# Optimization experiments

Hardware: AMD Instinct MI355X
Metric: run time of the kernel (lower is better)

The kernel has to match this reference:

```python
import jax, jax.numpy as jnp
import numpy as np


def setup_inputs() -> dict:
    key = jax.random.key(0)
    ks = jax.random.split(key, 7)
    B, T, H, O = 2048, 2048, 32, 2
    SCALE = 0.1  # keep gates out of deep saturation
    return {
        "x": jax.random.normal(ks[0], (B, T), dtype=jnp.float32),
        "w_ih": jax.random.normal(ks[1], (3 * H, 1), dtype=jnp.float32) * SCALE,
        "w_hh": jax.random.normal(ks[2], (3 * H, H), dtype=jnp.float32) * SCALE,
        "b_ih": jax.random.normal(ks[3], (3 * H,), dtype=jnp.float32) * SCALE,
        "b_hh": jax.random.normal(ks[4], (3 * H,), dtype=jnp.float32) * SCALE,
        "head_w": jax.random.normal(ks[5], (O, H), dtype=jnp.float32) * SCALE,
        "head_b": jax.random.normal(ks[6], (O,), dtype=jnp.float32) * SCALE,
    }


def reference(x, w_ih, w_hh, b_ih, b_hh, head_w, head_b):
    # x: [B, T] scalar time series (torch does x.unsqueeze(-1)).
    B, T = x.shape
    H = w_hh.shape[1]
    # Precompute input contributions to all 3 gates: [B, T, 3H]
    # (input_size == 1, so this is an outer product with w_ih[:, 0]).
    xg = x[:, :, None] * w_ih[:, 0] + b_ih
    xg_t = jnp.swapaxes(xg, 0, 1)  # [T, B, 3H] for scan

    def step(h, xg_step):
        gh = h @ w_hh.T + b_hh  # [B, 3H]
        xr, xz, xn = jnp.split(xg_step, 3, axis=-1)
        hr, hz, hn = jnp.split(gh, 3, axis=-1)
        r = jax.nn.sigmoid(xr + hr)
        z = jax.nn.sigmoid(xz + hz)
        n = jnp.tanh(xn + r * hn)
        h_new = (1.0 - z) * n + z * h
        return h_new, None

    h0 = jnp.zeros((B, H), dtype=x.dtype)
    hT, _ = jax.lax.scan(step, h0, xg_t)
    # head applied to last timestep's output (== final hidden state)
    return hT @ head_w.T + head_b
```

## Files before the change

### kernel.cpp

```cpp
#include <hip/hip_runtime.h>


typedef _Float16 f16x2 __attribute__((ext_vector_type(2)));

__device__ __forceinline__ float fdot2(int a, int b, float c) {
    return __builtin_amdgcn_fdot2(__builtin_bit_cast(f16x2, a),
                                  __builtin_bit_cast(f16x2, b), c, false);
}

__device__ __forceinline__ int pack_pair(float a, float b) {
    f16x2 p;
    p.x = (_Float16)a;
    p.y = (_Float16)b;
    return __builtin_bit_cast(int, p);
}

__global__ __launch_bounds__(64, 1)
void gru_scan_kernel(const float* __restrict__ x,
                     const float* __restrict__ w_ih,
                     const float* __restrict__ w_hh,
                     const float* __restrict__ b_ih,
                     const float* __restrict__ b_hh,
                     const float* __restrict__ head_w,
                     const float* __restrict__ head_b,
                     float* __restrict__ out,
                     int T)
{
    const int l = (int)threadIdx.x;
    const int g = l >> 5;
    const int j = l & 31;
    const int b = (int)blockIdx.x * 2 + g;

    __shared__ __align__(16) _Float16 h16[2][32];
    __shared__ float hf_s[2][32];
    __shared__ __align__(16) float x_s[2][2][32];

    const float NL2E  = -1.44269504088896f;
    const float P2L2E =  2.88539008177793f;

    int wR[16], wZ[16], wN[16];
    {
        const float* pR = w_hh + (     j) * 32;
        const float* pZ = w_hh + (32 + j) * 32;
        const float* pN = w_hh + (64 + j) * 32;
#pragma unroll
        for (int q = 0; q < 16; ++q) {
            wR[q] = pack_pair(NL2E  * pR[2*q], NL2E  * pR[2*q+1]);
            wZ[q] = pack_pair(NL2E  * pZ[2*q], NL2E  * pZ[2*q+1]);
            wN[q] = pack_pair(P2L2E * pN[2*q], P2L2E * pN[2*q+1]);
        }
    }
#pragma unroll
    for (int q = 0; q < 16; ++q) {
        asm volatile("" : "+v"(wR[q]), "+v"(wZ[q]), "+v"(wN[q]));
    }

    const float wihr = NL2E  * w_ih[j];
    const float wihz = NL2E  * w_ih[32 + j];
    const float wihn = P2L2E * w_ih[64 + j];
    const float br   = NL2E  * (b_ih[j]      + b_hh[j]);
    const float bz   = NL2E  * (b_ih[32 + j] + b_hh[32 + j]);
    const float bni  = P2L2E * b_ih[64 + j];
    const float bnh  = P2L2E * b_hh[64 + j];

    const float* xrow   = x + (size_t)b * (size_t)T;
    const int    nchunk = T >> 5;

    float h = 0.0f;
    h16[g][j]    = (_Float16)0.0f;
    x_s[g][0][j] = xrow[j];
    float xnext  = (nchunk > 1) ? xrow[32 + j] : 0.0f;
    __builtin_amdgcn_wave_barrier();

    const int4* hq = (const int4*)(&h16[g][0]);

    for (int c = 0; c < nchunk; ++c) {
        const int buf = c & 1;
        const float* xs = &x_s[g][buf][0];
#pragma unroll 4
        for (int s = 0; s < 32; ++s) {
            const float xv = xs[s];
            const int4 H0 = hq[0];
            const int4 H1 = hq[1];
            const int4 H2 = hq[2];
            const int4 H3 = hq[3];
            const float hm1 = h - 1.0f;

            float rA = fdot2(H0.x, wR[ 0], fmaf(xv, wihr, br));
            float rB = fdot2(H1.x, wR[ 4], 0.0f);
            float rC = fdot2(H2.x, wR[ 8], 0.0f);
            float rD = fdot2(H3.x, wR[12], 0.0f);
            rA = fdot2(H0.y, wR[ 1], rA); rB = fdot2(H1.y, wR[ 5], rB);
            rC = fdot2(H2.y, wR[ 9], rC); rD = fdot2(H3.y, wR[13], rD);
            rA = fdot2(H0.z, wR[ 2], rA); rB = fdot2(H1.z, wR[ 6], rB);
            rC = fdot2(H2.z, wR[10], rC); rD = fdot2(H3.z, wR[14], rD);
            rA = fdot2(H0.w, wR[ 3], rA); rB = fdot2(H1.w, wR[ 7], rB);
            rC = fdot2(H2.w, wR[11], rC); rD = fdot2(H3.w, wR[15], rD);
            const float er = __builtin_amdgcn_exp2f((rA + rB) + (rC + rD));
            const float r  = __builtin_amdgcn_rcpf(1.0f + er);

            float zA = fdot2(H0.x, wZ[ 0], fmaf(xv, wihz, bz));
            float zB = fdot2(H1.x, wZ[ 4], 0.0f);
            float zC = fdot2(H2.x, wZ[ 8], 0.0f);
            float zD = fdot2(H3.x, wZ[12], 0.0f);
            zA = fdot2(H0.y, wZ[ 1], zA); zB = fdot2(H1.y, wZ[ 5], zB);
            zC = fdot2(H2.y, wZ[ 9], zC); zD = fdot2(H3.y, wZ[13], zD);
            zA = fdot2(H0.z, wZ[ 2], zA); zB = fdot2(H1.z, wZ[ 6], zB);
            zC = fdot2(H2.z, wZ[10], zC); zD = fdot2(H3.z, wZ[14], zD);
            zA = fdot2(H0.w, wZ[ 3], zA); zB = fdot2(H1.w, wZ[ 7], zB);
            zC = fdot2(H2.w, wZ[11], zC); zD = fdot2(H3.w, wZ[15], zD);
            const float ez    = __builtin_amdgcn_exp2f((zA + zB) + (zC + zD));
            const float z     = __builtin_amdgcn_rcpf(1.0f + ez);
            const float m2omz = fmaf(2.0f, z, -2.0f);
            const float ohz   = fmaf(z, hm1, 1.0f);

            float nA = fdot2(H0.x, wN[ 0], bnh);
            float nB = fdot2(H1.x, wN[ 4], 0.0f);
            float nC = fdot2(H2.x, wN[ 8], 0.0f);
            float nD = fdot2(H3.x, wN[12], 0.0f);
            nA = fdot2(H0.y, wN[ 1], nA); nB = fdot2(H1.y, wN[ 5], nB);
            nC = fdot2(H2.y, wN[ 9], nC); nD = fdot2(H3.y, wN[13], nD);
            nA = fdot2(H0.z, wN[ 2], nA); nB = fdot2(H1.z, wN[ 6], nB);
            nC = fdot2(H2.z, wN[10], nC); nD = fdot2(H3.z, wN[14], nD);
            nA = fdot2(H0.w, wN[ 3], nA); nB = fdot2(H1.w, wN[ 7], nB);
            nC = fdot2(H2.w, wN[11], nC); nD = fdot2(H3.w, wN[15], nD);
            const float np = (nA + nB) + (nC + nD);
            const float u  = fmaf(r, np, fmaf(xv, wihn, bni));
            const float et = __builtin_amdgcn_exp2f(u);
            const float ti = __builtin_amdgcn_rcpf(1.0f + et);
            h = fmaf(m2omz, ti, ohz);

            __builtin_amdgcn_wave_barrier();
            h16[g][j] = (_Float16)h;
            __builtin_amdgcn_wave_barrier();
        }
        if (c + 1 < nchunk) {
            x_s[g][1 - buf][j] = xnext;
            if (c + 2 < nchunk) xnext = xrow[(c + 2) * 32 + j];
            __builtin_amdgcn_wave_barrier();
        }
    }

    hf_s[g][j] = h;
    __builtin_amdgcn_wave_barrier();
    if (l < 4) {
        const int g2 = l >> 1, o = l & 1;
        float acc = head_b[o];
        const float* hw = head_w + o * 32;
#pragma unroll
        for (int k = 0; k < 32; ++k) acc = fmaf(hf_s[g2][k], hw[k], acc);
        out[((int)blockIdx.x * 2 + g2) * 2 + o] = acc;
    }
}

extern "C" void kernel_launch(void* const* d_in, const int* in_sizes, int n_in,
                              void* d_out, int out_size, void* d_ws, size_t ws_size,
                              hipStream_t stream) {
    const float* x      = (const float*)d_in[0];
    const float* w_ih   = (const float*)d_in[1];
    const float* w_hh   = (const float*)d_in[2];
    const float* b_ih   = (const float*)d_in[3];
    const float* b_hh   = (const float*)d_in[4];
    const float* head_w = (const float*)d_in[5];
    const float* head_b = (const float*)d_in[6];
    float* out = (float*)d_out;

    const int B = out_size / 2;
    const int T = in_sizes[0] / B;

    dim3 grid(B / 2), block(64);
    hipLaunchKernelGGL(gru_scan_kernel, grid, block, 0, stream,
                       x, w_ih, w_hh, b_ih, b_hh, head_w, head_b, out, T);
}
```

Before: 526.3 us.

## Broadcast hidden state via permlane32_swap and DPP instead of LDS

Replaces the per-step LDS store and reload of the fp16 hidden state with register exchange. permlane32_swap pairs each lane's h with its partner half-wave, and a tree of DPP row permutes builds the 16 packed h pairs each lane needs. Lanes are remapped so the two batch elements interleave in 16-lane groups, and weight pairs are permuted at setup to match the DPP order. The aim is to cut LDS latency and the wave barriers from the serial recurrence critical path, at the cost of 16 extra DPP moves per step and fragile lane-mapping logic.

```diff
diff --git a/kernel.cpp b/kernel.cpp
--- a/kernel.cpp
+++ b/kernel.cpp
@@ -15,6 +15,11 @@
     return __builtin_bit_cast(int, p);
 }
 
+template<int CTRL>
+__device__ __forceinline__ int dppmov(int src) {
+    return __builtin_amdgcn_update_dpp(0, src, CTRL, 0xF, 0xF, true);
+}
+
 __global__ __launch_bounds__(64, 1)
 void gru_scan_kernel(const float* __restrict__ x,
                      const float* __restrict__ w_ih,
@@ -26,28 +31,40 @@
                      float* __restrict__ out,
                      int T)
 {
-    const int l = (int)threadIdx.x;
-    const int g = l >> 5;
-    const int j = l & 31;
-    const int b = (int)blockIdx.x * 2 + g;
+    const int l  = (int)threadIdx.x;
+    const int gg = (l >> 4) & 1;
+    const int m  = (l & 15) + ((l >> 5) << 4);
+    const int b  = (int)blockIdx.x * 2 + gg;
 
-    __shared__ __align__(16) _Float16 h16[2][32];
     __shared__ float hf_s[2][32];
     __shared__ __align__(16) float x_s[2][2][32];
+
+    bool lowfirst;
+    {
+        auto pr = __builtin_amdgcn_permlane32_swap((unsigned)l, (unsigned)l,
+                                                   false, false);
+        lowfirst = ((int)pr[0] == (l & 31));
+    }
 
     const float NL2E  = -1.44269504088896f;
     const float P2L2E =  2.88539008177793f;
 
+    constexpr int M[16] = {0,1,2,3,7,6,5,4,15,14,13,12,8,9,10,11};
+    const int c0 = l & 15;
+
     int wR[16], wZ[16], wN[16];
     {
-        const float* pR = w_hh + (     j) * 32;
-        const float* pZ = w_hh + (32 + j) * 32;
-        const float* pN = w_hh + (64 + j) * 32;
+        const float* pR = w_hh + (     m) * 32;
+        const float* pZ = w_hh + (32 + m) * 32;
+        const float* pN = w_hh + (64 + m) * 32;
 #pragma unroll
         for (int q = 0; q < 16; ++q) {
-            wR[q] = pack_pair(NL2E  * pR[2*q], NL2E  * pR[2*q+1]);
-            wZ[q] = pack_pair(NL2E  * pZ[2*q], NL2E  * pZ[2*q+1]);
-            wN[q] = pack_pair(P2L2E * pN[2*q], P2L2E * pN[2*q+1]);
+            const int cc  = c0 ^ M[q];
+            const int clo = lowfirst ? cc      : cc + 16;
+            const int chi = lowfirst ? cc + 16 : cc;
+            wR[q] = pack_pair(NL2E  * pR[clo], NL2E  * pR[chi]);
+            wZ[q] = pack_pair(NL2E  * pZ[clo], NL2E  * pZ[chi]);
+            wN[q] = pack_pair(P2L2E * pN[clo], P2L2E * pN[chi]);
         }
     }
 #pragma unroll
@@ -55,93 +72,95 @@
         asm volatile("" : "+v"(wR[q]), "+v"(wZ[q]), "+v"(wN[q]));
     }
 
-    const float wihr = NL2E  * w_ih[j];
-    const float wihz = NL2E  * w_ih[32 + j];
-    const float wihn = P2L2E * w_ih[64 + j];
-    const float br   = NL2E  * (b_ih[j]      + b_hh[j]);
-    const float bz   = NL2E  * (b_ih[32 + j] + b_hh[32 + j]);
-    const float bni  = P2L2E * b_ih[64 + j];
-    const float bnh  = P2L2E * b_hh[64 + j];
+    const float wihr = NL2E  * w_ih[m];
+    const float wihz = NL2E  * w_ih[32 + m];
+    const float wihn = P2L2E * w_ih[64 + m];
+    const float br   = NL2E  * (b_ih[m]      + b_hh[m]);
+    const float bz   = NL2E  * (b_ih[32 + m] + b_hh[32 + m]);
+    const float bni  = P2L2E * b_ih[64 + m];
+    const float bnh  = P2L2E * b_hh[64 + m];
 
     const float* xrow   = x + (size_t)b * (size_t)T;
     const int    nchunk = T >> 5;
 
     float h = 0.0f;
-    h16[g][j]    = (_Float16)0.0f;
-    x_s[g][0][j] = xrow[j];
-    float xnext  = (nchunk > 1) ? xrow[32 + j] : 0.0f;
+    x_s[gg][0][m] = xrow[m];
+    float xnext  = (nchunk > 1) ? xrow[32 + m] : 0.0f;
     __builtin_amdgcn_wave_barrier();
-
-    const int4* hq = (const int4*)(&h16[g][0]);
 
     for (int c = 0; c < nchunk; ++c) {
         const int buf = c & 1;
-        const float* xs = &x_s[g][buf][0];
+        const float* xs = &x_s[gg][buf][0];
 #pragma unroll 4
         for (int s = 0; s < 32; ++s) {
-            const float xv = xs[s];
-            const int4 H0 = hq[0];
-            const int4 H1 = hq[1];
-            const int4 H2 = hq[2];
-            const int4 H3 = hq[3];
+            const float xv  = xs[s];
             const float hm1 = h - 1.0f;
 
-            float rA = fdot2(H0.x, wR[ 0], fmaf(xv, wihr, br));
-            float rB = fdot2(H1.x, wR[ 4], 0.0f);
-            float rC = fdot2(H2.x, wR[ 8], 0.0f);
-            float rD = fdot2(H3.x, wR[12], 0.0f);
-            rA = fdot2(H0.y, wR[ 1], rA); rB = fdot2(H1.y, wR[ 5], rB);
-            rC = fdot2(H2.y, wR[ 9], rC); rD = fdot2(H3.y, wR[13], rD);
-            rA = fdot2(H0.z, wR[ 2], rA); rB = fdot2(H1.z, wR[ 6], rB);
-            rC = fdot2(H2.z, wR[10], rC); rD = fdot2(H3.z, wR[14], rD);
-            rA = fdot2(H0.w, wR[ 3], rA); rB = fdot2(H1.w, wR[ 7], rB);
-            rC = fdot2(H2.w, wR[11], rC); rD = fdot2(H3.w, wR[15], rD);
-            const float er = __builtin_amdgcn_exp2f((rA + rB) + (rC + rD));
+            const unsigned hf = (unsigned)__builtin_bit_cast(unsigned short,
+                                                             (_Float16)h);
+            auto sw = __builtin_amdgcn_permlane32_swap(hf, hf, false, false);
+            const int o0 = (int)sw[0];
+            const int o1 = (int)sw[1];
+            const int P0  = (o1 << 16) | o0;
+            const int P1  = dppmov<0xB1 >(P0);
+            const int P2  = dppmov<0x4E >(P0);
+            const int P3  = dppmov<0x4E >(P1);
+            const int P4  = dppmov<0x141>(P0);
+            const int P5  = dppmov<0x141>(P1);
+            const int P6  = dppmov<0x141>(P2);
+            const int P7  = dppmov<0x141>(P3);
+            const int P8  = dppmov<0x140>(P0);
+            const int P9  = dppmov<0x140>(P1);
+            const int P10 = dppmov<0x140>(P2);
+            const int P11 = dppmov<0x140>(P3);
+            const int P12 = dppmov<0x140>(P4);
+            const int P13 = dppmov<0x140>(P5);
+            const int P14 = dppmov<0x140>(P6);
+            const int P15 = dppmov<0x140>(P7);
+
+            float rA = fdot2(P0, wR[0], fmaf(xv, wihr, br));
+            float zA = fdot2(P0, wZ[0], fmaf(xv, wihz, bz));
+            float nA = fdot2(P0, wN[0], bnh);
+            float rB = fdot2(P8, wR[8], 0.0f);
+            float zB = fdot2(P8, wZ[8], 0.0f);
+            float nB = fdot2(P8, wN[8], 0.0f);
+            rA = fdot2(P1, wR[1], rA); zA = fdot2(P1, wZ[1], zA); nA = fdot2(P1, wN[1], nA);
+            rB = fdot2(P9, wR[9], rB); zB = fdot2(P9, wZ[9], zB); nB = fdot2(P9, wN[9], nB);
+            rA = fdot2(P2, wR[2], rA); zA = fdot2(P2, wZ[2], zA); nA = fdot2(P2, wN[2], nA);
+            rB = fdot2(P10, wR[10], rB); zB = fdot2(P10, wZ[10], zB); nB = fdot2(P10, wN[10], nB);
+            rA = fdot2(P3, wR[3], rA); zA = fdot2(P3, wZ[3], zA); nA = fdot2(P3, wN[3], nA);
+            rB = fdot2(P11, wR[11], rB); zB = fdot2(P11, wZ[11], zB); nB = fdot2(P11, wN[11], nB);
+            rA = fdot2(P4, wR[4], rA); zA = fdot2(P4, wZ[4], zA); nA = fdot2(P4, wN[4], nA);
+            rB = fdot2(P12, wR[12], rB); zB = fdot2(P12, wZ[12], zB); nB = fdot2(P12, wN[12], nB);
+            rA = fdot2(P5, wR[5], rA); zA = fdot2(P5, wZ[5], zA); nA = fdot2(P5, wN[5], nA);
+            rB = fdot2(P13, wR[13], rB); zB = fdot2(P13, wZ[13], zB); nB = fdot2(P13, wN[13], nB);
+            rA = fdot2(P6, wR[6], rA); zA = fdot2(P6, wZ[6], zA); nA = fdot2(P6, wN[6], nA);
+            rB = fdot2(P14, wR[14], rB); zB = fdot2(P14, wZ[14], zB); nB = fdot2(P14, wN[14], nB);
+            rA = fdot2(P7, wR[7], rA); zA = fdot2(P7, wZ[7], zA); nA = fdot2(P7, wN[7], nA);
+            rB = fdot2(P15, wR[15], rB); zB = fdot2(P15, wZ[15], zB); nB = fdot2(P15, wN[15], nB);
+
+            const float rp = rA + rB;
+            const float zp = zA + zB;
+            const float np = nA + nB;
+            const float er = __builtin_amdgcn_exp2f(rp);
+            const float ez = __builtin_amdgcn_exp2f(zp);
             const float r  = __builtin_amdgcn_rcpf(1.0f + er);
-
-            float zA = fdot2(H0.x, wZ[ 0], fmaf(xv, wihz, bz));
-            float zB = fdot2(H1.x, wZ[ 4], 0.0f);
-            float zC = fdot2(H2.x, wZ[ 8], 0.0f);
-            float zD = fdot2(H3.x, wZ[12], 0.0f);
-            zA = fdot2(H0.y, wZ[ 1], zA); zB = fdot2(H1.y, wZ[ 5], zB);
-            zC = fdot2(H2.y, wZ[ 9], zC); zD = fdot2(H3.y, wZ[13], zD);
-            zA = fdot2(H0.z, wZ[ 2], zA); zB = fdot2(H1.z, wZ[ 6], zB);
-            zC = fdot2(H2.z, wZ[10], zC); zD = fdot2(H3.z, wZ[14], zD);
-            zA = fdot2(H0.w, wZ[ 3], zA); zB = fdot2(H1.w, wZ[ 7], zB);
-            zC = fdot2(H2.w, wZ[11], zC); zD = fdot2(H3.w, wZ[15], zD);
-            const float ez    = __builtin_amdgcn_exp2f((zA + zB) + (zC + zD));
-            const float z     = __builtin_amdgcn_rcpf(1.0f + ez);
+            const float z  = __builtin_amdgcn_rcpf(1.0f + ez);
             const float m2omz = fmaf(2.0f, z, -2.0f);
             const float ohz   = fmaf(z, hm1, 1.0f);
-
-            float nA = fdot2(H0.x, wN[ 0], bnh);
-            float nB = fdot2(H1.x, wN[ 4], 0.0f);
-            float nC = fdot2(H2.x, wN[ 8], 0.0f);
-            float nD = fdot2(H3.x, wN[12], 0.0f);
-            nA = fdot2(H0.y, wN[ 1], nA); nB = fdot2(H1.y, wN[ 5], nB);
-            nC = fdot2(H2.y, wN[ 9], nC); nD = fdot2(H3.y, wN[13], nD);
-            nA = fdot2(H0.z, wN[ 2], nA); nB = fdot2(H1.z, wN[ 6], nB);
-            nC = fdot2(H2.z, wN[10], nC); nD = fdot2(H3.z, wN[14], nD);
-            nA = fdot2(H0.w, wN[ 3], nA); nB = fdot2(H1.w, wN[ 7], nB);
-            nC = fdot2(H2.w, wN[11], nC); nD = fdot2(H3.w, wN[15], nD);
-            const float np = (nA + nB) + (nC + nD);
             const float u  = fmaf(r, np, fmaf(xv, wihn, bni));
             const float et = __builtin_amdgcn_exp2f(u);
             const float ti = __builtin_amdgcn_rcpf(1.0f + et);
             h = fmaf(m2omz, ti, ohz);
-
-            __builtin_amdgcn_wave_barrier();
-            h16[g][j] = (_Float16)h;
-            __builtin_amdgcn_wave_barrier();
         }
         if (c + 1 < nchunk) {
-            x_s[g][1 - buf][j] = xnext;
-            if (c + 2 < nchunk) xnext = xrow[(c + 2) * 32 + j];
+            x_s[gg][1 - buf][m] = xnext;
+            if (c + 2 < nchunk) xnext = xrow[(c + 2) * 32 + m];
             __builtin_amdgcn_wave_barrier();
         }
     }
 
-    hf_s[g][j] = h;
+    hf_s[gg][m] = h;
     __builtin_amdgcn_wave_barrier();
     if (l < 4) {
         const int g2 = l >> 1, o = l & 1;
```

Result: faster. 449.6 us, median of 2 (-14.6%).
